# Kernel optimization log

Measured on AMD Instinct MI355X. Metric: run time of the kernel, lower is better.

Reference implementation:

```python
import jax, jax.numpy as jnp
import numpy as np

B, L, D, H, A, NLAYERS, P = 16, 512, 768, 4, 100, 2, 3
DK = A // H  # 25
EPS = 1e-6


def setup_inputs() -> dict:
    key = jax.random.key(0)
    ks = jax.random.split(key, 20)
    s = 0.02
    return {
        "sequence_output": jax.random.normal(ks[0], (B, L, D), jnp.float32),
        "syntax_matrix": jax.random.normal(ks[1], (B, H, L, L), jnp.float32),
        # LayerNorm params
        "ln_a": jnp.ones((D,), jnp.float32),
        "ln_b": jnp.zeros((D,), jnp.float32),
        # Wxx: bert_dim -> attdim
        "Wxx_w": jax.random.normal(ks[2], (A, D), jnp.float32) * s,
        "Wxx_b": jnp.zeros((A,), jnp.float32),
        # attention q/k projections (attdim -> attdim)
        "q_w": jax.random.normal(ks[3], (A, A), jnp.float32) * s,
        "q_b": jnp.zeros((A,), jnp.float32),
        "k_w": jax.random.normal(ks[4], (A, A), jnp.float32) * s,
        "k_b": jnp.zeros((A,), jnp.float32),
        # W: attdim -> attdim
        "W_w": jax.random.normal(ks[5], (A, A), jnp.float32) * s,
        "W_b": jnp.zeros((A,), jnp.float32),
        # Wx: (H + 2*attdim) -> H
        "Wx_w": jax.random.normal(ks[6], (H, H + 2 * A), jnp.float32) * s,
        "Wx_b": jnp.zeros((H,), jnp.float32),
        # aggregate_W: attdim*(layers+1) -> attdim
        "agg_w": jax.random.normal(ks[7], (A, A * (NLAYERS + 1)), jnp.float32) * s,
        "agg_b": jnp.zeros((A,), jnp.float32),
        # classifier: 100 -> polarities_dim
        "cls_w": jax.random.normal(ks[8], (P, A), jnp.float32) * s,
        "cls_b": jnp.zeros((P,), jnp.float32),
        # masks (ints)
        "mask_ids": jnp.ones((B, L), jnp.int32),
        "src_mask": jnp.ones((B, L), jnp.int32),
    }


def reference(sequence_output, syntax_matrix, ln_a, ln_b, Wxx_w, Wxx_b,
              q_w, q_b, k_w, k_b, W_w, W_b, Wx_w, Wx_b,
              agg_w, agg_b, cls_w, cls_b, mask_ids, src_mask):
    # custom LayerNorm: torch.std is unbiased (ddof=1)
    mean = sequence_output.mean(-1, keepdims=True)
    std = jnp.std(sequence_output, axis=-1, ddof=1, keepdims=True)
    seq = ln_a * (sequence_output - mean) / (std + EPS) + ln_b

    # Wxx projection to attdim (dropout = identity in eval)
    x = seq @ Wxx_w.T + Wxx_b  # [B, L, A]

    # multi-head attention producing adjacency [B, H, L, L]
    q = (x @ q_w.T + q_b).reshape(B, L, H, DK).transpose(0, 2, 1, 3)
    k = (x @ k_w.T + k_b).reshape(B, L, H, DK).transpose(0, 2, 1, 3)
    scores = jnp.einsum('bhid,bhjd->bhij', q, k) / jnp.sqrt(jnp.float32(DK))
    key_mask = src_mask[:, None, None, :]  # [B,1,1,L]
    scores = jnp.where(key_mask == 0, jnp.float32(-1e9), scores)
    scores = scores + syntax_matrix
    adj = jax.nn.softmax(scores, axis=-1)  # [B, H, L, L]

    # split Wx into its adjacency / node-j / node-i blocks so the [B,L,L,H+2A]
    # concat tensor is never materialized (edge MLP is linear => decomposable)
    Aw = Wx_w[:, :H]            # [H, H]
    B1 = Wx_w[:, H:H + A]       # [H, A] applied to x[b, j]
    B2 = Wx_w[:, H + A:]        # [H, A] applied to x[b, i]

    x_g = x
    layer_list = [x]
    for i in range(NLAYERS):
        # Ax = mean over heads of adj_h @ x  (x identical per head)
        Ax = jnp.einsum('bhij,bjd->bid', adj, x_g) / H
        x_g = jax.nn.relu(Ax @ W_w.T + W_b)  # [B, L, A]
        layer_list.append(x_g)
        # edge update: edge[b,g,i,j] = sum_h Aw[g,h]*adj[b,h,i,j]
        e_adj = jnp.einsum('bhij,gh->bgij', adj, Aw)  # [B, H, L, L]
        u = jnp.einsum('bjd,gd->bgj', x_g, B1)        # node1 (index j)
        v = jnp.einsum('bid,gd->bgi', x_g, B2)        # node2 (index i)
        adj = e_adj + u[:, :, None, :] + v[:, :, :, None] + Wx_b[None, :, None, None]

    feats = jnp.concatenate(layer_list, axis=-1)          # [B, L, A*(NLAYERS+1)]
    node = jax.nn.relu(feats @ agg_w.T + agg_b)           # [B, L, A]

    valid_len = jnp.clip(mask_ids.sum(axis=1), 1, None).astype(node.dtype)[:, None]
    pooled = node.sum(axis=1) / valid_len                 # [B, A]
    logits = pooled @ cls_w.T + cls_b                     # [B, P]
    return logits
```

## Files before the change

### kernel.cpp

```cpp
#include <hip/hip_runtime.h>

#define B_ 16
#define L_ 512
#define D_ 768
#define H_ 4
#define A_ 100
#define DK_ 25
#define P_ 3
#define XP_ 128

typedef unsigned int u32_t;
typedef const u32_t __attribute__((address_space(1)))* gas_t;
typedef u32_t __attribute__((address_space(3)))* las_t;
__device__ __forceinline__ void dma16(const float* g, float* l) {
    __builtin_amdgcn_global_load_lds((gas_t)g, (las_t)l, 16, 0, 0);
}

__global__ __launch_bounds__(256) void k_wprep(const float* __restrict__ Wxx_w,
                                               const float* __restrict__ ln_a,
                                               float* __restrict__ wT)
{
    const int idx = blockIdx.x * 256 + threadIdx.x;
    const int d = idx >> 7, a = idx & 127;
    wT[idx] = (a < A_) ? ln_a[d] * Wxx_w[(size_t)a * D_ + d] : 0.f;
}

__global__ __launch_bounds__(128) void k_vecprep(const float* __restrict__ Wxx_w,
                                                 const float* __restrict__ ln_a,
                                                 const float* __restrict__ ln_b,
                                                 const float* __restrict__ Wxx_b,
                                                 float* __restrict__ colsum,
                                                 float* __restrict__ basev)
{
    const int a = threadIdx.x;
    float cs = 0.f, bs = 0.f;
    if (a < A_) {
        const float* wr = Wxx_w + (size_t)a * D_;
        for (int d = 0; d < D_; ++d) {
            const float w = wr[d];
            cs += ln_a[d] * w;
            bs += ln_b[d] * w;
        }
        bs += Wxx_b[a];
    }
    colsum[a] = (a < A_) ? cs : 0.f;
    basev[a]  = (a < A_) ? bs : 0.f;
}

__global__ __launch_bounds__(256) void k_aggprep(const float* __restrict__ agg_w,
                                                 float* __restrict__ aggT)
{
    const int idx = blockIdx.x * 256 + threadIdx.x;
    const int n = idx & 127, k = (idx >> 7) % A_, c = idx / (128 * A_);
    aggT[idx] = (n < A_) ? agg_w[(size_t)n * (3 * A_) + c * A_ + k] : 0.f;
}

__global__ __launch_bounds__(256) void k_qkprep(const float* __restrict__ q_w,
                                                const float* __restrict__ k_w,
                                                float* __restrict__ qkT)
{
    const int idx = blockIdx.x * 256 + threadIdx.x;
    const int n = idx & 255, k = idx >> 8;
    const int half = n >> 7, a = n & 127;
    const float* w = half ? k_w : q_w;
    qkT[idx] = (a < A_) ? w[(size_t)a * A_ + k] : 0.f;
}

__global__ __launch_bounds__(256) void k_wprep2(const float* __restrict__ W_w,
                                                float* __restrict__ WT)
{
    const int idx = blockIdx.x * 256 + threadIdx.x;
    const int n = idx & 127, k = idx >> 7;
    WT[idx] = (n < A_) ? W_w[(size_t)n * A_ + k] : 0.f;
}

__global__ __launch_bounds__(256) void k_lnx(
    const float* __restrict__ seq, const float* __restrict__ wT,
    const float* __restrict__ colsum, const float* __restrict__ basev,
    float* __restrict__ xp)
{
    __shared__ float ss[2][32][32];
    __shared__ float ws[2][32][128];
    __shared__ float mean_s[32], rd_s[32];
    const int tid = threadIdx.x;
    const int row0 = blockIdx.x * 32;
    const int wv = tid >> 6, lane = tid & 63;

    for (int rr = 0; rr < 8; ++rr) {
        const int r = wv * 8 + rr;
        const float4* src = (const float4*)(seq + (size_t)(row0 + r) * D_);
        float4 a = src[lane], b = src[lane + 64], c = src[lane + 128];
        float s = a.x + a.y + a.z + a.w + b.x + b.y + b.z + b.w + c.x + c.y + c.z + c.w;
        #pragma unroll
        for (int o = 32; o; o >>= 1) s += __shfl_xor(s, o);
        const float m = s * (1.0f / 768.0f);
        float q = (a.x-m)*(a.x-m) + (a.y-m)*(a.y-m) + (a.z-m)*(a.z-m) + (a.w-m)*(a.w-m)
                + (b.x-m)*(b.x-m) + (b.y-m)*(b.y-m) + (b.z-m)*(b.z-m) + (b.w-m)*(b.w-m)
                + (c.x-m)*(c.x-m) + (c.y-m)*(c.y-m) + (c.z-m)*(c.z-m) + (c.w-m)*(c.w-m);
        #pragma unroll
        for (int o = 32; o; o >>= 1) q += __shfl_xor(q, o);
        if (lane == 0) {
            mean_s[r] = m;
            rd_s[r] = 1.0f / (sqrtf(q * (1.0f / 767.0f)) + 1e-6f);
        }
    }

    const int c4 = tid & 31, rg = tid >> 5;
    float4 acc[4];
    #pragma unroll
    for (int i = 0; i < 4; ++i) { acc[i].x = acc[i].y = acc[i].z = acc[i].w = 0.f; }

    const int sr = tid >> 3, sk = (tid & 7) * 4;
    dma16(seq + (size_t)(row0 + sr) * D_ + sk, &ss[0][0][0] + tid * 4);
    #pragma unroll
    for (int t = 0; t < 4; ++t) {
        const int idx = tid + t * 256;
        dma16(wT + idx * 4, &ws[0][0][0] + idx * 4);
    }
    __syncthreads();

    for (int kc = 0; kc < 24; ++kc) {
        const int cur = kc & 1;
        if (kc < 23) {
            dma16(seq + (size_t)(row0 + sr) * D_ + (kc + 1) * 32 + sk,
                  &ss[cur ^ 1][0][0] + tid * 4);
            #pragma unroll
            for (int t = 0; t < 4; ++t) {
                const int idx = tid + t * 256;
                dma16(wT + (size_t)(kc + 1) * 4096 + idx * 4, &ws[cur ^ 1][0][0] + idx * 4);
            }
        }
        #pragma unroll
        for (int k = 0; k < 32; k += 4) {
            float4 sv[4];
            #pragma unroll
            for (int i = 0; i < 4; ++i) sv[i] = *(float4*)&ss[cur][rg * 4 + i][k];
            #pragma unroll
            for (int j = 0; j < 4; ++j) {
                float4 w4 = *(float4*)&ws[cur][k + j][c4 * 4];
                #pragma unroll
                for (int i = 0; i < 4; ++i) {
                    const float sj = ((float*)&sv[i])[j];
                    acc[i].x += sj * w4.x; acc[i].y += sj * w4.y;
                    acc[i].z += sj * w4.z; acc[i].w += sj * w4.w;
                }
            }
        }
        __syncthreads();
    }

    const float4 cs4 = ((const float4*)colsum)[c4];
    const float4 bs4 = ((const float4*)basev)[c4];
    #pragma unroll
    for (int i = 0; i < 4; ++i) {
        const int r = rg * 4 + i;
        const float m = mean_s[r], rd = rd_s[r];
        float4 o;
        o.x = rd * (acc[i].x - m * cs4.x) + bs4.x;
        o.y = rd * (acc[i].y - m * cs4.y) + bs4.y;
        o.z = rd * (acc[i].z - m * cs4.z) + bs4.z;
        o.w = rd * (acc[i].w - m * cs4.w) + bs4.w;
        *(float4*)(xp + (size_t)(row0 + r) * XP_ + c4 * 4) = o;
    }
}

__global__ __launch_bounds__(256) void k_qkg(
    const float* __restrict__ xp, const float* __restrict__ qkT,
    const float* __restrict__ q_b, const float* __restrict__ k_b,
    float* __restrict__ qt, float* __restrict__ kt)
{
    __shared__ float ss[32][104];
    __shared__ float ws[A_][128];
    const int tid = threadIdx.x;
    const int row0 = blockIdx.x * 32;
    const int half = blockIdx.y;
    const int c4 = tid & 31, rg = tid >> 5;

    for (int idx = tid; idx < 32 * 25; idx += 256) {
        const int r = idx / 25, k4 = idx % 25;
        *(float4*)&ss[r][k4 * 4] = *(const float4*)(xp + (size_t)(row0 + r) * XP_ + k4 * 4);
    }
    for (int idx = tid; idx < A_ * 32; idx += 256) {
        const int k = idx >> 5, cc = idx & 31;
        *(float4*)&ws[k][cc * 4] = *(const float4*)(qkT + (size_t)k * 256 + half * 128 + cc * 4);
    }
    __syncthreads();

    float4 acc[4];
    #pragma unroll
    for (int i = 0; i < 4; ++i) { acc[i].x = acc[i].y = acc[i].z = acc[i].w = 0.f; }
    #pragma unroll 5
    for (int k = 0; k < A_; k += 4) {
        float4 sv[4];
        #pragma unroll
        for (int i = 0; i < 4; ++i) sv[i] = *(float4*)&ss[rg * 4 + i][k];
        #pragma unroll
        for (int j = 0; j < 4; ++j) {
            float4 w4 = *(float4*)&ws[k + j][c4 * 4];
            #pragma unroll
            for (int i = 0; i < 4; ++i) {
                const float sj = ((float*)&sv[i])[j];
                acc[i].x += sj * w4.x; acc[i].y += sj * w4.y;
                acc[i].z += sj * w4.z; acc[i].w += sj * w4.w;
            }
        }
    }

    if (c4 < 25) {
        const float4 bias = ((const float4*)(half ? k_b : q_b))[c4];
        float* dst = half ? kt : qt;
        #pragma unroll
        for (int i = 0; i < 4; ++i) {
            float4 o;
            o.x = acc[i].x + bias.x; o.y = acc[i].y + bias.y;
            o.z = acc[i].z + bias.z; o.w = acc[i].w + bias.w;
            *(float4*)(dst + (size_t)(row0 + rg * 4 + i) * A_ + c4 * 4) = o;
        }
    }
}

__global__ __launch_bounds__(256) void k_sgemm(
    const float* __restrict__ qt, const float* __restrict__ kt,
    const float* __restrict__ syn, const int* __restrict__ src_mask,
    float* __restrict__ es)
{
    __shared__ float qs[DK_][64];
    __shared__ float ks[DK_][64];
    __shared__ int ms[64];
    const int tid = threadIdx.x;
    const int bh = blockIdx.z;
    const int b = bh >> 2, h = bh & 3;
    const int i0 = blockIdx.x * 64, j0 = blockIdx.y * 64;
    const float* qbase = qt + ((size_t)b * L_ + i0) * A_ + h * DK_;
    const float* kbase = kt + ((size_t)b * L_ + j0) * A_ + h * DK_;
    {
        const int r = tid >> 2, c = tid & 3;
        #pragma unroll
        for (int k = 0; k < 7; ++k) {
            const int d = c + 4 * k;
            if (d < DK_) {
                qs[d][r] = qbase[(size_t)r * A_ + d];
                ks[d][r] = kbase[(size_t)r * A_ + d];
            }
        }
        if (tid < 64) ms[tid] = src_mask[b * L_ + j0 + tid];
    }
    __syncthreads();
    const int ty = tid >> 4, tx = tid & 15;
    float acc[4][4] = {};
    #pragma unroll 5
    for (int d = 0; d < DK_; ++d) {
        float4 qv = *(const float4*)&qs[d][ty * 4];
        float4 kv = *(const float4*)&ks[d][tx * 4];
        const float q[4] = {qv.x, qv.y, qv.z, qv.w};
        const float kk[4] = {kv.x, kv.y, kv.z, kv.w};
        #pragma unroll
        for (int ii = 0; ii < 4; ++ii)
            #pragma unroll
            for (int jj = 0; jj < 4; ++jj)
                acc[ii][jj] += q[ii] * kk[jj];
    }
    const int irow = i0 + ty * 4, jcol = j0 + tx * 4;
    const int m0 = ms[tx * 4], m1 = ms[tx * 4 + 1], m2 = ms[tx * 4 + 2], m3 = ms[tx * 4 + 3];
    #pragma unroll
    for (int ii = 0; ii < 4; ++ii) {
        const size_t o = ((size_t)bh * L_ + irow + ii) * L_ + jcol;
        float4 sv = *(const float4*)(syn + o);
        float4 w;
        w.x = (m0 ? acc[ii][0] * 0.2f : -1e9f) + sv.x;
        w.y = (m1 ? acc[ii][1] * 0.2f : -1e9f) + sv.y;
        w.z = (m2 ? acc[ii][2] * 0.2f : -1e9f) + sv.z;
        w.w = (m3 ? acc[ii][3] * 0.2f : -1e9f) + sv.w;
        *(float4*)(es + o) = w;
    }
}

__global__ __launch_bounds__(256) void k_softmax(
    const float* __restrict__ Wx_w, float* __restrict__ es)
{
    __shared__ float ps[H_][L_];
    __shared__ float cs[H_];
    const int tid = threadIdx.x, r = blockIdx.x;
    const int b = r >> 9, i = r & 511;
    const int h = tid >> 6, lane = tid & 63;
    if (tid < H_) cs[tid] = Wx_w[tid] + Wx_w[204 + tid] + Wx_w[408 + tid] + Wx_w[612 + tid];
    float* row = es + (((size_t)(b * H_ + h)) * L_ + i) * L_;
    float4 v0 = ((const float4*)row)[lane];
    float4 v1 = ((const float4*)row)[lane + 64];
    float mx = fmaxf(fmaxf(fmaxf(v0.x, v0.y), fmaxf(v0.z, v0.w)),
                     fmaxf(fmaxf(v1.x, v1.y), fmaxf(v1.z, v1.w)));
    #pragma unroll
    for (int o = 32; o; o >>= 1) mx = fmaxf(mx, __shfl_xor(mx, o));
    float4 e0, e1;
    e0.x = __expf(v0.x - mx); e0.y = __expf(v0.y - mx);
    e0.z = __expf(v0.z - mx); e0.w = __expf(v0.w - mx);
    e1.x = __expf(v1.x - mx); e1.y = __expf(v1.y - mx);
    e1.z = __expf(v1.z - mx); e1.w = __expf(v1.w - mx);
    float sum = e0.x + e0.y + e0.z + e0.w + e1.x + e1.y + e1.z + e1.w;
    #pragma unroll
    for (int o = 32; o; o >>= 1) sum += __shfl_xor(sum, o);
    const float inv = 1.0f / sum;
    e0.x *= inv; e0.y *= inv; e0.z *= inv; e0.w *= inv;
    e1.x *= inv; e1.y *= inv; e1.z *= inv; e1.w *= inv;
    *(float4*)&ps[h][lane * 4] = e0;
    *(float4*)&ps[h][(lane + 64) * 4] = e1;
    __syncthreads();
    float* arow = es + (((size_t)(b * H_ + 0)) * L_ + i) * L_;
    float* wrow = es + (((size_t)(b * H_ + 1)) * L_ + i) * L_;
    const int t = tid & 127;
    float4 p0 = *(float4*)&ps[0][t * 4];
    float4 p1 = *(float4*)&ps[1][t * 4];
    float4 p2 = *(float4*)&ps[2][t * 4];
    float4 p3 = *(float4*)&ps[3][t * 4];
    if (tid < 128) {
        float4 o;
        o.x = p0.x + p1.x + p2.x + p3.x;
        o.y = p0.y + p1.y + p2.y + p3.y;
        o.z = p0.z + p1.z + p2.z + p3.z;
        o.w = p0.w + p1.w + p2.w + p3.w;
        *(float4*)(arow + t * 4) = o;
    } else {
        const float c0 = cs[0], c1 = cs[1], c2 = cs[2], c3 = cs[3];
        float4 o;
        o.x = c0 * p0.x + c1 * p1.x + c2 * p2.x + c3 * p3.x;
        o.y = c0 * p0.y + c1 * p1.y + c2 * p2.y + c3 * p3.y;
        o.z = c0 * p0.z + c1 * p1.z + c2 * p2.z + c3 * p3.z;
        o.w = c0 * p0.w + c1 * p1.w + c2 * p2.w + c3 * p3.w;
        *(float4*)(wrow + t * 4) = o;
    }
}

template<int LAYER2>
__global__ __launch_bounds__(256) void k_axg(
    const float* __restrict__ adj, const float* __restrict__ xp,
    const float* __restrict__ S, const float* __restrict__ T,
    const float* __restrict__ Vv, const float* __restrict__ Wx_b,
    float* __restrict__ axb)
{
    __shared__ float ss[2][32][32];
    __shared__ float ws[2][32][128];
    const int tid = threadIdx.x;
    const int row0 = blockIdx.x * 32;
    const int b = row0 >> 9, i0 = row0 & 511;
    const float* adjb = adj + (size_t)b * 4 * L_ * L_;
    const float* xpb = xp + (size_t)b * L_ * XP_;
    const int c4 = tid & 31, rg = tid >> 5;
    float4 acc[4];
    #pragma unroll
    for (int i = 0; i < 4; ++i) { acc[i].x = acc[i].y = acc[i].z = acc[i].w = 0.f; }

    const int sr = tid >> 3, sk = (tid & 7) * 4;
    dma16(adjb + (size_t)(i0 + sr) * L_ + sk, &ss[0][0][0] + tid * 4);
    #pragma unroll
    for (int t = 0; t < 4; ++t) {
        const int idx = tid + t * 256;
        dma16(xpb + idx * 4, &ws[0][0][0] + idx * 4);
    }
    __syncthreads();

    for (int kc = 0; kc < 16; ++kc) {
        const int cur = kc & 1;
        if (kc < 15) {
            dma16(adjb + (size_t)(i0 + sr) * L_ + (kc + 1) * 32 + sk,
                  &ss[cur ^ 1][0][0] + tid * 4);
            #pragma unroll
            for (int t = 0; t < 4; ++t) {
                const int idx = tid + t * 256;
                dma16(xpb + (size_t)(kc + 1) * 4096 + idx * 4, &ws[cur ^ 1][0][0] + idx * 4);
            }
        }
        #pragma unroll
        for (int k = 0; k < 32; k += 4) {
            float4 sv[4];
            #pragma unroll
            for (int i = 0; i < 4; ++i) sv[i] = *(float4*)&ss[cur][rg * 4 + i][k];
            #pragma unroll
            for (int j = 0; j < 4; ++j) {
                float4 w4 = *(float4*)&ws[cur][k + j][c4 * 4];
                #pragma unroll
                for (int i = 0; i < 4; ++i) {
                    const float sj = ((float*)&sv[i])[j];
                    acc[i].x += sj * w4.x; acc[i].y += sj * w4.y;
                    acc[i].z += sj * w4.z; acc[i].w += sj * w4.w;
                }
            }
        }
        __syncthreads();
    }

    float wb = 0.f;
    float4 Sv = {0.f, 0.f, 0.f, 0.f}, Tv = {0.f, 0.f, 0.f, 0.f};
    if (LAYER2) {
        wb = Wx_b[0] + Wx_b[1] + Wx_b[2] + Wx_b[3];
        if (c4 < 25) {
            Sv = ((const float4*)(S + b * A_))[c4];
            Tv = ((const float4*)(T + b * A_))[c4];
        }
    }
    #pragma unroll
    for (int i = 0; i < 4; ++i) {
        const int grow = row0 + rg * 4 + i;
        const float vv = LAYER2 ? (Vv[grow] + wb) : 0.f;
        float4 o;
        o.x = (acc[i].x + Sv.x + vv * Tv.x) * 0.25f;
        o.y = (acc[i].y + Sv.y + vv * Tv.y) * 0.25f;
        o.z = (acc[i].z + Sv.z + vv * Tv.z) * 0.25f;
        o.w = (acc[i].w + Sv.w + vv * Tv.w) * 0.25f;
        *(float4*)(axb + (size_t)grow * XP_ + c4 * 4) = o;
    }
}

__global__ __launch_bounds__(256) void k_xw(
    const float* __restrict__ axb, const float* __restrict__ WT,
    const float* __restrict__ W_b, float* __restrict__ xout)
{
    __shared__ float ss[32][104];
    __shared__ float ws[A_][128];
    const int tid = threadIdx.x;
    const int row0 = blockIdx.x * 32;
    const int c4 = tid & 31, rg = tid >> 5;

    for (int idx = tid; idx < 32 * 25; idx += 256) {
        const int r = idx / 25, k4 = idx % 25;
        *(float4*)&ss[r][k4 * 4] = *(const float4*)(axb + (size_t)(row0 + r) * XP_ + k4 * 4);
    }
    for (int idx = tid; idx < A_ * 32; idx += 256) {
        const int k = idx >> 5, cc = idx & 31;
        *(float4*)&ws[k][cc * 4] = *(const float4*)(WT + (size_t)k * 128 + cc * 4);
    }
    __syncthreads();

    float4 acc[4];
    #pragma unroll
    for (int i = 0; i < 4; ++i) { acc[i].x = acc[i].y = acc[i].z = acc[i].w = 0.f; }
    #pragma unroll 5
    for (int k = 0; k < A_; k += 4) {
        float4 sv[4];
        #pragma unroll
        for (int i = 0; i < 4; ++i) sv[i] = *(float4*)&ss[rg * 4 + i][k];
        #pragma unroll
        for (int j = 0; j < 4; ++j) {
            float4 w4 = *(float4*)&ws[k + j][c4 * 4];
            #pragma unroll
            for (int i = 0; i < 4; ++i) {
                const float sj = ((float*)&sv[i])[j];
                acc[i].x += sj * w4.x; acc[i].y += sj * w4.y;
                acc[i].z += sj * w4.z; acc[i].w += sj * w4.w;
            }
        }
    }

    float4 bias = {0.f, 0.f, 0.f, 0.f};
    if (c4 < 25) bias = ((const float4*)W_b)[c4];
    #pragma unroll
    for (int i = 0; i < 4; ++i) {
        float4 o;
        o.x = fmaxf(acc[i].x + bias.x, 0.f); o.y = fmaxf(acc[i].y + bias.y, 0.f);
        o.z = fmaxf(acc[i].z + bias.z, 0.f); o.w = fmaxf(acc[i].w + bias.w, 0.f);
        *(float4*)(xout + (size_t)(row0 + rg * 4 + i) * XP_ + c4 * 4) = o;
    }
}

__global__ __launch_bounds__(256) void k_extras(
    const float* __restrict__ x1, const float* __restrict__ Wx_w,
    float* __restrict__ Vv, float* __restrict__ T, float* __restrict__ S,
    float* __restrict__ pooled)
{
    __shared__ float b1s[A_], b2s[A_], Ul[L_];
    const int tid = threadIdx.x, b = blockIdx.x;
    if (tid < A_) {
        float s1 = 0.f, s2 = 0.f;
        #pragma unroll
        for (int g = 0; g < H_; ++g) {
            s1 += Wx_w[g * 204 + 4 + tid];
            s2 += Wx_w[g * 204 + 104 + tid];
        }
        b1s[tid] = s1; b2s[tid] = s2;
        pooled[b * A_ + tid] = 0.f;
    }
    __syncthreads();
    for (int j = tid; j < L_; j += 256) {
        const float* xr = x1 + ((size_t)b * L_ + j) * XP_;
        float u = 0.f, v = 0.f;
        #pragma unroll 4
        for (int c = 0; c < A_; ++c) { float xv = xr[c]; u += xv * b1s[c]; v += xv * b2s[c]; }
        Ul[j] = u;
        Vv[b * L_ + j] = v;
    }
    __syncthreads();
    if (tid < A_) {
        float t = 0.f, s = 0.f;
        for (int j = 0; j < L_; ++j) {
            float xv = x1[((size_t)b * L_ + j) * XP_ + tid];
            t += xv; s += Ul[j] * xv;
        }
        T[b * A_ + tid] = t; S[b * A_ + tid] = s;
    }
}

__global__ __launch_bounds__(256) void k_nodepool(
    const float* __restrict__ x, const float* __restrict__ x1, const float* __restrict__ x2,
    const float* __restrict__ aggT, const float* __restrict__ agg_b,
    float* __restrict__ pooled)
{
    __shared__ float ss[32][104];
    __shared__ float ws[A_][128];
    const int tid = threadIdx.x;
    const int row0 = blockIdx.x * 32;
    const int b = row0 >> 9;
    const int c4 = tid & 31, rg = tid >> 5;
    float4 acc[4];
    #pragma unroll
    for (int i = 0; i < 4; ++i) { acc[i].x = acc[i].y = acc[i].z = acc[i].w = 0.f; }

    for (int c = 0; c < 3; ++c) {
        const float* src = (c == 0) ? x : (c == 1) ? x1 : x2;
        for (int idx = tid; idx < 32 * 25; idx += 256) {
            const int r = idx / 25, k4 = idx % 25;
            *(float4*)&ss[r][k4 * 4] =
                *(const float4*)(src + (size_t)(row0 + r) * XP_ + k4 * 4);
        }
        for (int idx = tid; idx < A_ * 32; idx += 256) {
            const int k = idx >> 5, cc = idx & 31;
            *(float4*)&ws[k][cc * 4] =
                *(const float4*)(aggT + ((size_t)c * A_ + k) * 128 + cc * 4);
        }
        __syncthreads();
        #pragma unroll 5
        for (int k = 0; k < A_; k += 4) {
            float4 sv[4];
            #pragma unroll
            for (int i = 0; i < 4; ++i) sv[i] = *(float4*)&ss[rg * 4 + i][k];
            #pragma unroll
            for (int j = 0; j < 4; ++j) {
                float4 w4 = *(float4*)&ws[k + j][c4 * 4];
                #pragma unroll
                for (int i = 0; i < 4; ++i) {
                    const float sj = ((float*)&sv[i])[j];
                    acc[i].x += sj * w4.x; acc[i].y += sj * w4.y;
                    acc[i].z += sj * w4.z; acc[i].w += sj * w4.w;
                }
            }
        }
        __syncthreads();
    }

    float4 bias = {0.f, 0.f, 0.f, 0.f};
    if (c4 < 25) bias = ((const float4*)agg_b)[c4];
    float4 rs = {0.f, 0.f, 0.f, 0.f};
    #pragma unroll
    for (int i = 0; i < 4; ++i) {
        rs.x += fmaxf(acc[i].x + bias.x, 0.f);
        rs.y += fmaxf(acc[i].y + bias.y, 0.f);
        rs.z += fmaxf(acc[i].z + bias.z, 0.f);
        rs.w += fmaxf(acc[i].w + bias.w, 0.f);
    }
    float* red = &ss[0][0];
    __syncthreads();
    *(float4*)&red[rg * 128 + c4 * 4] = rs;
    __syncthreads();
    if (rg == 0 && c4 < 25) {
        float4 tot = {0.f, 0.f, 0.f, 0.f};
        #pragma unroll
        for (int g = 0; g < 8; ++g) {
            float4 v = *(float4*)&red[g * 128 + c4 * 4];
            tot.x += v.x; tot.y += v.y; tot.z += v.z; tot.w += v.w;
        }
        atomicAdd(&pooled[b * A_ + c4 * 4 + 0], tot.x);
        atomicAdd(&pooled[b * A_ + c4 * 4 + 1], tot.y);
        atomicAdd(&pooled[b * A_ + c4 * 4 + 2], tot.z);
        atomicAdd(&pooled[b * A_ + c4 * 4 + 3], tot.w);
    }
}

__global__ __launch_bounds__(64) void k_logits(
    const float* __restrict__ pooled, const float* __restrict__ cls_w,
    const float* __restrict__ cls_b, const int* __restrict__ mask_ids,
    float* __restrict__ out)
{
    const int tid = threadIdx.x;
    if (tid < B_ * P_) {
        const int b = tid / P_, p = tid % P_;
        int vs = 0;
        for (int l = 0; l < L_; ++l) vs += mask_ids[b * L_ + l];
        float inv = 1.0f / (float)max(vs, 1);
        float acc = cls_b[p];
        #pragma unroll 4
        for (int a = 0; a < A_; ++a) acc += (pooled[b * A_ + a] * inv) * cls_w[p * A_ + a];
        out[b * P_ + p] = acc;
    }
}

extern "C" void kernel_launch(void* const* d_in, const int* in_sizes, int n_in,
                              void* d_out, int out_size, void* d_ws, size_t ws_size,
                              hipStream_t stream) {
    const float* seq    = (const float*)d_in[0];
    const float* syn    = (const float*)d_in[1];
    const float* ln_a   = (const float*)d_in[2];
    const float* ln_b   = (const float*)d_in[3];
    const float* Wxx_w  = (const float*)d_in[4];
    const float* Wxx_b  = (const float*)d_in[5];
    const float* q_w    = (const float*)d_in[6];
    const float* q_b    = (const float*)d_in[7];
    const float* k_w    = (const float*)d_in[8];
    const float* k_b    = (const float*)d_in[9];
    const float* W_w    = (const float*)d_in[10];
    const float* W_b    = (const float*)d_in[11];
    const float* Wx_w   = (const float*)d_in[12];
    const float* Wx_b   = (const float*)d_in[13];
    const float* agg_w  = (const float*)d_in[14];
    const float* agg_b  = (const float*)d_in[15];
    const float* cls_w  = (const float*)d_in[16];
    const float* cls_b  = (const float*)d_in[17];
    const int* mask_ids = (const int*)d_in[18];
    const int* src_mask = (const int*)d_in[19];
    float* out = (float*)d_out;

    float* ws = (float*)d_ws;
    size_t off = 0;
    float* xp     = ws + off; off += (size_t)B_ * L_ * XP_;
    float* x1p    = ws + off; off += (size_t)B_ * L_ * XP_;
    float* x2p    = ws + off; off += (size_t)B_ * L_ * XP_;
    float* axb    = ws + off; off += (size_t)B_ * L_ * XP_;
    float* qt     = ws + off; off += (size_t)B_ * L_ * A_;
    float* kt     = ws + off; off += (size_t)B_ * L_ * A_;
    float* es     = ws + off; off += (size_t)B_ * H_ * L_ * L_;
    float* Vv     = ws + off; off += (size_t)B_ * L_;
    float* T      = ws + off; off += (size_t)B_ * A_;
    float* S      = ws + off; off += (size_t)B_ * A_;
    float* pooled = ws + off; off += (size_t)B_ * A_;
    float* wT     = ws + off; off += (size_t)D_ * 128;
    float* aggT   = ws + off; off += (size_t)3 * A_ * 128;
    float* qkT    = ws + off; off += (size_t)A_ * 256;
    float* WT     = ws + off; off += (size_t)A_ * 128;
    float* colsum = ws + off; off += 128;
    float* basev  = ws + off; off += 128;

    k_wprep<<<(D_ * 128) / 256, 256, 0, stream>>>(Wxx_w, ln_a, wT);
    k_vecprep<<<1, 128, 0, stream>>>(Wxx_w, ln_a, ln_b, Wxx_b, colsum, basev);
    k_aggprep<<<(3 * A_ * 128) / 256, 256, 0, stream>>>(agg_w, aggT);
    k_qkprep<<<(A_ * 256) / 256, 256, 0, stream>>>(q_w, k_w, qkT);
    k_wprep2<<<(A_ * 128) / 256, 256, 0, stream>>>(W_w, WT);
    k_lnx<<<(B_ * L_) / 32, 256, 0, stream>>>(seq, wT, colsum, basev, xp);
    k_qkg<<<dim3((B_ * L_) / 32, 2), 256, 0, stream>>>(xp, qkT, q_b, k_b, qt, kt);
    k_sgemm<<<dim3(8, 8, B_ * H_), 256, 0, stream>>>(qt, kt, syn, src_mask, es);
    k_softmax<<<B_ * L_, 256, 0, stream>>>(Wx_w, es);
    k_axg<0><<<(B_ * L_) / 32, 256, 0, stream>>>(es, xp, nullptr, nullptr, nullptr, nullptr, axb);
    k_xw<<<(B_ * L_) / 32, 256, 0, stream>>>(axb, WT, W_b, x1p);
    k_extras<<<B_, 256, 0, stream>>>(x1p, Wx_w, Vv, T, S, pooled);
    k_axg<1><<<(B_ * L_) / 32, 256, 0, stream>>>(es + (size_t)L_ * L_, x1p, S, T, Vv, Wx_b, axb);
    k_xw<<<(B_ * L_) / 32, 256, 0, stream>>>(axb, WT, W_b, x2p);
    k_nodepool<<<(B_ * L_) / 32, 256, 0, stream>>>(xp, x1p, x2p, aggT, agg_b, pooled);
    k_logits<<<1, 64, 0, stream>>>(pooled, cls_w, cls_b, mask_ids, out);
}
```

Baseline: 413.2 us.

## Halve row tiles, drop LDS DMA double-buffering, fuse LayerNorm stats into GEMM

Three kernels (k_lnx, k_axg, k_xw) move from 32-row tiles with 256 threads to 16-row tiles with 128 threads, which doubles the grid size. The global_load_lds double-buffered prefetch is replaced with plain single-buffered register-to-LDS loads plus a barrier per chunk. In k_lnx the separate mean/variance pass is removed: row sums and sums of squares are accumulated while the GEMM reads the tile, and variance uses the one-pass formula. The aim is more blocks in flight and no redundant read of the input rows. The cost is less overlap between loads and compute, twice as many reloads of the weight tile overall, and some numerical risk from the one-pass variance.

New measurement: 464.2 us. +12.3%, slower.

```diff
diff --git a/kernel.cpp b/kernel.cpp
--- a/kernel.cpp
+++ b/kernel.cpp
@@ -9,13 +9,6 @@
 #define P_ 3
 #define XP_ 128
 
-typedef unsigned int u32_t;
-typedef const u32_t __attribute__((address_space(1)))* gas_t;
-typedef u32_t __attribute__((address_space(3)))* las_t;
-__device__ __forceinline__ void dma16(const float* g, float* l) {
-    __builtin_amdgcn_global_load_lds((gas_t)g, (las_t)l, 16, 0, 0);
-}
-
 __global__ __launch_bounds__(256) void k_wprep(const float* __restrict__ Wxx_w,
                                                const float* __restrict__ ln_a,
                                                float* __restrict__ wT)
@@ -74,70 +67,49 @@
     WT[idx] = (n < A_) ? W_w[(size_t)n * A_ + k] : 0.f;
 }
 
-__global__ __launch_bounds__(256) void k_lnx(
+__global__ __launch_bounds__(128) void k_lnx(
     const float* __restrict__ seq, const float* __restrict__ wT,
     const float* __restrict__ colsum, const float* __restrict__ basev,
     float* __restrict__ xp)
 {
-    __shared__ float ss[2][32][32];
-    __shared__ float ws[2][32][128];
-    __shared__ float mean_s[32], rd_s[32];
+    __shared__ float ss[16][36];
+    __shared__ float ws[32][128];
     const int tid = threadIdx.x;
-    const int row0 = blockIdx.x * 32;
-    const int wv = tid >> 6, lane = tid & 63;
-
-    for (int rr = 0; rr < 8; ++rr) {
-        const int r = wv * 8 + rr;
-        const float4* src = (const float4*)(seq + (size_t)(row0 + r) * D_);
-        float4 a = src[lane], b = src[lane + 64], c = src[lane + 128];
-        float s = a.x + a.y + a.z + a.w + b.x + b.y + b.z + b.w + c.x + c.y + c.z + c.w;
-        #pragma unroll
-        for (int o = 32; o; o >>= 1) s += __shfl_xor(s, o);
-        const float m = s * (1.0f / 768.0f);
-        float q = (a.x-m)*(a.x-m) + (a.y-m)*(a.y-m) + (a.z-m)*(a.z-m) + (a.w-m)*(a.w-m)
-                + (b.x-m)*(b.x-m) + (b.y-m)*(b.y-m) + (b.z-m)*(b.z-m) + (b.w-m)*(b.w-m)
-                + (c.x-m)*(c.x-m) + (c.y-m)*(c.y-m) + (c.z-m)*(c.z-m) + (c.w-m)*(c.w-m);
-        #pragma unroll
-        for (int o = 32; o; o >>= 1) q += __shfl_xor(q, o);
-        if (lane == 0) {
-            mean_s[r] = m;
-            rd_s[r] = 1.0f / (sqrtf(q * (1.0f / 767.0f)) + 1e-6f);
-        }
-    }
-
+    const int row0 = blockIdx.x * 16;
     const int c4 = tid & 31, rg = tid >> 5;
+
     float4 acc[4];
+    float rsum[4] = {0.f, 0.f, 0.f, 0.f};
+    float rsq[4]  = {0.f, 0.f, 0.f, 0.f};
     #pragma unroll
     for (int i = 0; i < 4; ++i) { acc[i].x = acc[i].y = acc[i].z = acc[i].w = 0.f; }
 
-    const int sr = tid >> 3, sk = (tid & 7) * 4;
-    dma16(seq + (size_t)(row0 + sr) * D_ + sk, &ss[0][0][0] + tid * 4);
-    #pragma unroll
-    for (int t = 0; t < 4; ++t) {
-        const int idx = tid + t * 256;
-        dma16(wT + idx * 4, &ws[0][0][0] + idx * 4);
-    }
-    __syncthreads();
-
     for (int kc = 0; kc < 24; ++kc) {
-        const int cur = kc & 1;
-        if (kc < 23) {
-            dma16(seq + (size_t)(row0 + sr) * D_ + (kc + 1) * 32 + sk,
-                  &ss[cur ^ 1][0][0] + tid * 4);
-            #pragma unroll
-            for (int t = 0; t < 4; ++t) {
-                const int idx = tid + t * 256;
-                dma16(wT + (size_t)(kc + 1) * 4096 + idx * 4, &ws[cur ^ 1][0][0] + idx * 4);
-            }
-        }
-        #pragma unroll
+        {
+            const int r = tid >> 3, k4 = tid & 7;
+            *(float4*)&ss[r][k4 * 4] =
+                *(const float4*)(seq + (size_t)(row0 + r) * D_ + kc * 32 + k4 * 4);
+        }
+        #pragma unroll
+        for (int t = 0; t < 8; ++t) {
+            const int idx = tid + t * 128;
+            const int k = idx >> 5, cc = idx & 31;
+            *(float4*)&ws[k][cc * 4] = *(const float4*)(wT + (size_t)(kc * 32 + k) * 128 + cc * 4);
+        }
+        __syncthreads();
+        #pragma unroll 2
         for (int k = 0; k < 32; k += 4) {
             float4 sv[4];
             #pragma unroll
-            for (int i = 0; i < 4; ++i) sv[i] = *(float4*)&ss[cur][rg * 4 + i][k];
+            for (int i = 0; i < 4; ++i) {
+                sv[i] = *(float4*)&ss[rg * 4 + i][k];
+                rsum[i] += sv[i].x + sv[i].y + sv[i].z + sv[i].w;
+                rsq[i]  += sv[i].x * sv[i].x + sv[i].y * sv[i].y
+                         + sv[i].z * sv[i].z + sv[i].w * sv[i].w;
+            }
             #pragma unroll
             for (int j = 0; j < 4; ++j) {
-                float4 w4 = *(float4*)&ws[cur][k + j][c4 * 4];
+                float4 w4 = *(float4*)&ws[k + j][c4 * 4];
                 #pragma unroll
                 for (int i = 0; i < 4; ++i) {
                     const float sj = ((float*)&sv[i])[j];
@@ -153,14 +125,15 @@
     const float4 bs4 = ((const float4*)basev)[c4];
     #pragma unroll
     for (int i = 0; i < 4; ++i) {
-        const int r = rg * 4 + i;
-        const float m = mean_s[r], rd = rd_s[r];
+        const float m = rsum[i] * (1.0f / 768.0f);
+        const float var = (rsq[i] - 768.0f * m * m) * (1.0f / 767.0f);
+        const float rd = 1.0f / (sqrtf(var) + 1e-6f);
         float4 o;
         o.x = rd * (acc[i].x - m * cs4.x) + bs4.x;
         o.y = rd * (acc[i].y - m * cs4.y) + bs4.y;
         o.z = rd * (acc[i].z - m * cs4.z) + bs4.z;
         o.w = rd * (acc[i].w - m * cs4.w) + bs4.w;
-        *(float4*)(xp + (size_t)(row0 + r) * XP_ + c4 * 4) = o;
+        *(float4*)(xp + (size_t)(row0 + rg * 4 + i) * XP_ + c4 * 4) = o;
     }
 }
 
@@ -331,16 +304,16 @@
 }
 
 template<int LAYER2>
-__global__ __launch_bounds__(256) void k_axg(
+__global__ __launch_bounds__(128) void k_axg(
     const float* __restrict__ adj, const float* __restrict__ xp,
     const float* __restrict__ S, const float* __restrict__ T,
     const float* __restrict__ Vv, const float* __restrict__ Wx_b,
     float* __restrict__ axb)
 {
-    __shared__ float ss[2][32][32];
-    __shared__ float ws[2][32][128];
+    __shared__ float ss[16][36];
+    __shared__ float ws[32][128];
     const int tid = threadIdx.x;
-    const int row0 = blockIdx.x * 32;
+    const int row0 = blockIdx.x * 16;
     const int b = row0 >> 9, i0 = row0 & 511;
     const float* adjb = adj + (size_t)b * 4 * L_ * L_;
     const float* xpb = xp + (size_t)b * L_ * XP_;
@@ -349,34 +322,28 @@
     #pragma unroll
     for (int i = 0; i < 4; ++i) { acc[i].x = acc[i].y = acc[i].z = acc[i].w = 0.f; }
 
-    const int sr = tid >> 3, sk = (tid & 7) * 4;
-    dma16(adjb + (size_t)(i0 + sr) * L_ + sk, &ss[0][0][0] + tid * 4);
-    #pragma unroll
-    for (int t = 0; t < 4; ++t) {
-        const int idx = tid + t * 256;
-        dma16(xpb + idx * 4, &ws[0][0][0] + idx * 4);
-    }
-    __syncthreads();
-
     for (int kc = 0; kc < 16; ++kc) {
-        const int cur = kc & 1;
-        if (kc < 15) {
-            dma16(adjb + (size_t)(i0 + sr) * L_ + (kc + 1) * 32 + sk,
-                  &ss[cur ^ 1][0][0] + tid * 4);
-            #pragma unroll
-            for (int t = 0; t < 4; ++t) {
-                const int idx = tid + t * 256;
-                dma16(xpb + (size_t)(kc + 1) * 4096 + idx * 4, &ws[cur ^ 1][0][0] + idx * 4);
-            }
-        }
-        #pragma unroll
+        {
+            const int r = tid >> 3, k4 = tid & 7;
+            *(float4*)&ss[r][k4 * 4] =
+                *(const float4*)(adjb + (size_t)(i0 + r) * L_ + kc * 32 + k4 * 4);
+        }
+        #pragma unroll
+        for (int t = 0; t < 8; ++t) {
+            const int idx = tid + t * 128;
+            const int k = idx >> 5, cc = idx & 31;
+            *(float4*)&ws[k][cc * 4] =
+                *(const float4*)(xpb + (size_t)(kc * 32 + k) * XP_ + cc * 4);
+        }
+        __syncthreads();
+        #pragma unroll 2
         for (int k = 0; k < 32; k += 4) {
             float4 sv[4];
             #pragma unroll
-            for (int i = 0; i < 4; ++i) sv[i] = *(float4*)&ss[cur][rg * 4 + i][k];
+            for (int i = 0; i < 4; ++i) sv[i] = *(float4*)&ss[rg * 4 + i][k];
             #pragma unroll
             for (int j = 0; j < 4; ++j) {
-                float4 w4 = *(float4*)&ws[cur][k + j][c4 * 4];
+                float4 w4 = *(float4*)&ws[k + j][c4 * 4];
                 #pragma unroll
                 for (int i = 0; i < 4; ++i) {
                     const float sj = ((float*)&sv[i])[j];
@@ -410,21 +377,21 @@
     }
 }
 
-__global__ __launch_bounds__(256) void k_xw(
+__global__ __launch_bounds__(128) void k_xw(
     const float* __restrict__ axb, const float* __restrict__ WT,
     const float* __restrict__ W_b, float* __restrict__ xout)
 {
-    __shared__ float ss[32][104];
+    __shared__ float ss[16][104];
     __shared__ float ws[A_][128];
     const int tid = threadIdx.x;
-    const int row0 = blockIdx.x * 32;
+    const int row0 = blockIdx.x * 16;
     const int c4 = tid & 31, rg = tid >> 5;
 
-    for (int idx = tid; idx < 32 * 25; idx += 256) {
+    for (int idx = tid; idx < 16 * 25; idx += 128) {
         const int r = idx / 25, k4 = idx % 25;
         *(float4*)&ss[r][k4 * 4] = *(const float4*)(axb + (size_t)(row0 + r) * XP_ + k4 * 4);
     }
-    for (int idx = tid; idx < A_ * 32; idx += 256) {
+    for (int idx = tid; idx < A_ * 32; idx += 128) {
         const int k = idx >> 5, cc = idx & 31;
         *(float4*)&ws[k][cc * 4] = *(const float4*)(WT + (size_t)k * 128 + cc * 4);
     }
@@ -641,15 +608,15 @@
     k_aggprep<<<(3 * A_ * 128) / 256, 256, 0, stream>>>(agg_w, aggT);
     k_qkprep<<<(A_ * 256) / 256, 256, 0, stream>>>(q_w, k_w, qkT);
     k_wprep2<<<(A_ * 128) / 256, 256, 0, stream>>>(W_w, WT);
-    k_lnx<<<(B_ * L_) / 32, 256, 0, stream>>>(seq, wT, colsum, basev, xp);
+    k_lnx<<<(B_ * L_) / 16, 128, 0, stream>>>(seq, wT, colsum, basev, xp);
     k_qkg<<<dim3((B_ * L_) / 32, 2), 256, 0, stream>>>(xp, qkT, q_b, k_b, qt, kt);
     k_sgemm<<<dim3(8, 8, B_ * H_), 256, 0, stream>>>(qt, kt, syn, src_mask, es);
     k_softmax<<<B_ * L_, 256, 0, stream>>>(Wx_w, es);
-    k_axg<0><<<(B_ * L_) / 32, 256, 0, stream>>>(es, xp, nullptr, nullptr, nullptr, nullptr, axb);
-    k_xw<<<(B_ * L_) / 32, 256, 0, stream>>>(axb, WT, W_b, x1p);
+    k_axg<0><<<(B_ * L_) / 16, 128, 0, stream>>>(es, xp, nullptr, nullptr, nullptr, nullptr, axb);
+    k_xw<<<(B_ * L_) / 16, 128, 0, stream>>>(axb, WT, W_b, x1p);
     k_extras<<<B_, 256, 0, stream>>>(x1p, Wx_w, Vv, T, S, pooled);
-    k_axg<1><<<(B_ * L_) / 32, 256, 0, stream>>>(es + (size_t)L_ * L_, x1p, S, T, Vv, Wx_b, axb);
-    k_xw<<<(B_ * L_) / 32, 256, 0, stream>>>(axb, WT, W_b, x2p);
+    k_axg<1><<<(B_ * L_) / 16, 128, 0, stream>>>(es + (size_t)L_ * L_, x1p, S, T, Vv, Wx_b, axb);
+    k_xw<<<(B_ * L_) / 16, 128, 0, stream>>>(axb, WT, W_b, x2p);
     k_nodepool<<<(B_ * L_) / 32, 256, 0, stream>>>(xp, x1p, x2p, aggT, agg_b, pooled);
     k_logits<<<1, 64, 0, stream>>>(pooled, cls_w, cls_b, mask_ids, out);
 }
```
